# Performance work log

Measured on AMD Instinct MI355X. Metric: run time of the kernel, lower is better.

The kernel has to match this reference:

```python
import jax, jax.numpy as jnp
import numpy as np

N, E = 100000, 1600000
D_IN, D_H, D_OUT = 32, 64, 1


def _init_linear(key, fan_in, fan_out):
    k1, k2 = jax.random.split(key)
    lim = 1.0 / np.sqrt(fan_in)
    w = jax.random.uniform(k1, (fan_in, fan_out), minval=-lim, maxval=lim, dtype=jnp.float32)
    b = jax.random.uniform(k2, (fan_out,), minval=-lim, maxval=lim, dtype=jnp.float32)
    return w, b


def setup_inputs() -> dict:
    key = jax.random.key(0)
    ks = jax.random.split(key, 8)
    x = jax.random.normal(ks[0], (N, D_IN), dtype=jnp.float32)
    edge_index = jax.random.randint(ks[1], (2, E), 0, N, dtype=jnp.int64)
    w1_rel, b1 = _init_linear(ks[2], D_IN, D_H)
    w1_root, _ = _init_linear(ks[3], D_IN, D_H)
    w2_rel, b2 = _init_linear(ks[4], D_H, D_H)
    w2_root, _ = _init_linear(ks[5], D_H, D_H)
    w3_rel, b3 = _init_linear(ks[6], D_H, D_OUT)
    w3_root, _ = _init_linear(ks[7], D_H, D_OUT)
    return {
        "x": x,
        "w1_rel": w1_rel, "b1": b1, "w1_root": w1_root,
        "w2_rel": w2_rel, "b2": b2, "w2_root": w2_root,
        "w3_rel": w3_rel, "b3": b3, "w3_root": w3_root,
        "edge_index": edge_index,
    }


def _graph_conv(x, edge_index, w_rel, b_rel, w_root):
    # PyG GraphConv: out_i = W_rel @ (sum_{j->i} x_j) + b_rel + W_root @ x_i
    src, dst = edge_index[0], edge_index[1]
    agg = jax.ops.segment_sum(x[src], dst, num_segments=x.shape[0])  # [N, d]
    return agg @ w_rel + b_rel + x @ w_root


def reference(x, w1_rel, b1, w1_root, w2_rel, b2, w2_root, w3_rel, b3, w3_root, edge_index):
    # Dropout is inactive in eval mode (F.dropout with training=False is identity).
    h = jax.nn.relu(_graph_conv(x, edge_index, w1_rel, b1, w1_root))
    h = jax.nn.relu(_graph_conv(h, edge_index, w2_rel, b2, w2_root))
    out = _graph_conv(h, edge_index, w3_rel, b3, w3_root)
    return out.reshape(-1)  # [N], since output_dim == 1
```

## Files before the change

kernel.cpp:

```cpp
#include <hip/hip_runtime.h>
#include <hip/hip_fp16.h>

typedef _Float16 f16x8 __attribute__((ext_vector_type(8)));
typedef float    f32x4 __attribute__((ext_vector_type(4)));

constexpr int DIN = 32;
constexpr int DH  = 64;
constexpr int NBSHIFT = 8;
constexpr int TILE_A  = 4096;


__global__ __launch_bounds__(256) void k_zero512(int* __restrict__ p) {
  p[threadIdx.x] = 0;
  p[256 + threadIdx.x] = 0;
}

__global__ __launch_bounds__(256) void k_chist(
    const int* __restrict__ dst, int* __restrict__ ch, int E, int nbuckets) {
  __shared__ int hist[512];
  long long t0 = (long long)blockIdx.x * TILE_A;
  int cnt = (int)min((long long)TILE_A, (long long)E - t0);
  for (int i = threadIdx.x; i < nbuckets; i += 256) hist[i] = 0;
  __syncthreads();
  for (int r = threadIdx.x; r < cnt; r += 256)
    atomicAdd(&hist[dst[t0 + r] >> NBSHIFT], 1);
  __syncthreads();
  for (int i = threadIdx.x; i < nbuckets; i += 256)
    if (hist[i]) atomicAdd(&ch[i], hist[i]);
}

__global__ __launch_bounds__(256) void k_cscan(
    const int* __restrict__ ch, int* __restrict__ cb, int* __restrict__ bcur,
    int nbuckets, int E) {
  __shared__ int ts[256];
  int i0 = threadIdx.x * 2, i1 = i0 + 1;
  int v0 = (i0 < nbuckets) ? ch[i0] : 0;
  int v1 = (i1 < nbuckets) ? ch[i1] : 0;
  int s = v0 + v1;
  ts[threadIdx.x] = s;
  __syncthreads();
  for (int off = 1; off < 256; off <<= 1) {
    int val = (threadIdx.x >= off) ? ts[threadIdx.x - off] : 0;
    __syncthreads();
    ts[threadIdx.x] += val;
    __syncthreads();
  }
  int ex = ts[threadIdx.x] - s;
  if (i0 < nbuckets) { cb[i0] = ex;      bcur[i0] = ex; }
  if (i1 < nbuckets) { cb[i1] = ex + v0; bcur[i1] = ex + v0; }
  if (threadIdx.x == 255) cb[nbuckets] = E;
}

__global__ __launch_bounds__(256) void k_binA(
    const int* __restrict__ src, const int* __restrict__ dst,
    int* __restrict__ bcur, unsigned* __restrict__ bin,
    int E, int nbuckets) {
  __shared__ int hist[512];
  __shared__ int base[512];
  long long t0 = (long long)blockIdx.x * TILE_A;
  int cnt = (int)min((long long)TILE_A, (long long)E - t0);
  for (int i = threadIdx.x; i < nbuckets; i += 256) hist[i] = 0;
  __syncthreads();
  for (int r = threadIdx.x; r < cnt; r += 256)
    atomicAdd(&hist[dst[t0 + r] >> NBSHIFT], 1);
  __syncthreads();
  for (int i = threadIdx.x; i < nbuckets; i += 256) {
    int c = hist[i];
    base[i] = c ? atomicAdd(&bcur[i], c) : 0;
    hist[i] = 0;
  }
  __syncthreads();
  for (int r = threadIdx.x; r < cnt; r += 256) {
    int d = dst[t0 + r];
    int s = src[t0 + r];
    int b = d >> NBSHIFT;
    int off = atomicAdd(&hist[b], 1);
    bin[base[b] + off] = ((unsigned)(d & 255) << 17) | (unsigned)s;
  }
}

__global__ __launch_bounds__(256) void k_fillB(
    const unsigned* __restrict__ bin, const int* __restrict__ cb,
    int* __restrict__ rp, int* __restrict__ ssrc, int n, int E) {
  __shared__ int deg[256];
  __shared__ int ts[256];
  __shared__ int cur[256];
  int b = blockIdx.x;
  int nbase = b << NBSHIFT;
  int nn = min(256, n - nbase);
  int ebeg = cb[b], eend = cb[b + 1];
  deg[threadIdx.x] = 0;
  __syncthreads();
  for (int e = ebeg + (int)threadIdx.x; e < eend; e += 256)
    atomicAdd(&deg[bin[e] >> 17], 1);
  __syncthreads();
  int d = deg[threadIdx.x];
  ts[threadIdx.x] = d;
  __syncthreads();
  for (int off = 1; off < 256; off <<= 1) {
    int val = (threadIdx.x >= off) ? ts[threadIdx.x - off] : 0;
    __syncthreads();
    ts[threadIdx.x] += val;
    __syncthreads();
  }
  int pref = ts[threadIdx.x] - d;
  if ((int)threadIdx.x < nn) {
    rp[nbase + threadIdx.x] = ebeg + pref;
    cur[threadIdx.x] = ebeg + pref;
  }
  if (b == 0 && threadIdx.x == 0) rp[n] = E;
  __syncthreads();
  for (int e = ebeg + (int)threadIdx.x; e < eend; e += 256) {
    unsigned u = bin[e];
    int dlow = (int)(u >> 17);
    int s = (int)(u & 0x1FFFF);
    int pos = atomicAdd(&cur[dlow], 1);
    ssrc[pos] = s;
  }
}


__global__ __launch_bounds__(256) void k_tohalf(
    const float2* __restrict__ in, __half2* __restrict__ f1, int n2) {
  int i = blockIdx.x * 256 + threadIdx.x;
  if (i >= n2) return;
  float2 v = in[i];
  int node = i >> 4, f2 = i & 15;
  f1[(size_t)node * 32 + f2] = __floats2half2_rn(v.x, v.y);
}

template<int LOGG, int LDH8, int OFFR8, int OFFW8>
__global__ __launch_bounds__(256) void k_gather(
    const f16x8* __restrict__ feat, const int* __restrict__ rp,
    const int* __restrict__ ssrc, f16x8* __restrict__ outp, int n) {
  int t = blockIdx.x * 256 + threadIdx.x;
  int node = t >> LOGG;
  int f8 = t & ((1 << LOGG) - 1);
  if (node >= n) return;
  int beg = rp[node], end = rp[node + 1];
  float acc[8];
#pragma unroll
  for (int j = 0; j < 8; ++j) acc[j] = 0.f;
  int e = beg;
  for (; e + 3 < end; e += 4) {
    int s0 = ssrc[e];
    int s1 = ssrc[e + 1];
    int s2 = ssrc[e + 2];
    int s3 = ssrc[e + 3];
    f16x8 v0 = feat[(size_t)s0 * LDH8 + OFFR8 + f8];
    f16x8 v1 = feat[(size_t)s1 * LDH8 + OFFR8 + f8];
    f16x8 v2 = feat[(size_t)s2 * LDH8 + OFFR8 + f8];
    f16x8 v3 = feat[(size_t)s3 * LDH8 + OFFR8 + f8];
#pragma unroll
    for (int j = 0; j < 8; ++j) {
      acc[j] += (float)v0[j];
      acc[j] += (float)v1[j];
      acc[j] += (float)v2[j];
      acc[j] += (float)v3[j];
    }
  }
  for (; e < end; ++e) {
    f16x8 v = feat[(size_t)ssrc[e] * LDH8 + OFFR8 + f8];
#pragma unroll
    for (int j = 0; j < 8; ++j) acc[j] += (float)v[j];
  }
  f16x8 r;
#pragma unroll
  for (int j = 0; j < 8; ++j) r[j] = (_Float16)acc[j];
  outp[(size_t)node * LDH8 + OFFW8 + f8] = r;
}


__global__ __launch_bounds__(256) void k_prepw1(
    const float* __restrict__ w_rel, const float* __restrict__ w_root,
    __half* __restrict__ wf) {
  int u = blockIdx.x * 256 + threadIdx.x;
  if (u >= 512) return;
  int lane = u & 63, kt = (u >> 6) & 1, mt = u >> 7;
  int out = 16 * mt + (lane & 15);
  int kb = 32 * kt + (lane >> 4) * 8;
  union { uint4 q; __half h[8]; } pk;
#pragma unroll
  for (int j = 0; j < 8; ++j) {
    int k = kb + j;
    float w = (k < 32) ? w_root[k * DH + out] : w_rel[(k - 32) * DH + out];
    pk.h[j] = __float2half(w);
  }
  *(uint4*)(wf + (size_t)u * 8) = pk.q;
}

__global__ __launch_bounds__(256) void k_prepw2(
    const float* __restrict__ w_rel, const float* __restrict__ w_root,
    __half* __restrict__ wf) {
  int u = blockIdx.x * 256 + threadIdx.x;
  if (u >= 1024) return;
  int lane = u & 63, kt = (u >> 6) & 3, mt = u >> 8;
  int out = 16 * mt + (lane & 15);
  int kb = 32 * kt + (lane >> 4) * 8;
  union { uint4 q; __half h[8]; } pk;
#pragma unroll
  for (int j = 0; j < 8; ++j) {
    int k = kb + j;
    float w = (k < 64) ? w_rel[k * DH + out] : w_root[(k - 64) * DH + out];
    pk.h[j] = __float2half(w);
  }
  *(uint4*)(wf + (size_t)u * 8) = pk.q;
}

__global__ __launch_bounds__(256) void k_l1mfma(
    const _Float16* __restrict__ F1, const _Float16* __restrict__ WF,
    const float* __restrict__ b1, _Float16* __restrict__ F2, int n) {
  int lane = threadIdx.x & 63;
  int wv = (blockIdx.x * 256 + threadIdx.x) >> 6;
  int nb = wv * 16;
  if (nb >= n) return;
  int node = nb + (lane & 15);
  int nodeld = min(node, n - 1);
  const _Float16* fp = F1 + (size_t)nodeld * 64 + (lane >> 4) * 8;
  f16x8 bf[2];
#pragma unroll
  for (int kt = 0; kt < 2; ++kt) bf[kt] = *(const f16x8*)(fp + kt * 32);
  const f16x8* ap = (const f16x8*)WF + lane;
  f32x4 acc[4];
#pragma unroll
  for (int mt = 0; mt < 4; ++mt) acc[mt] = (f32x4)(0.f);
#pragma unroll
  for (int mt = 0; mt < 4; ++mt)
#pragma unroll
    for (int kt = 0; kt < 2; ++kt)
      acc[mt] = __builtin_amdgcn_mfma_f32_16x16x32_f16(
          ap[(mt * 2 + kt) * 64], bf[kt], acc[mt], 0, 0, 0);
  if (node >= n) return;
  int jb = (lane >> 4) * 4;
  _Float16* op = F2 + (size_t)node * 128 + 64 + jb;
#pragma unroll
  for (int mt = 0; mt < 4; ++mt) {
    f32x4 vb = *(const f32x4*)(b1 + 16 * mt + jb);
    union { uint2 u; _Float16 h[4]; } pk;
#pragma unroll
    for (int r = 0; r < 4; ++r)
      pk.h[r] = (_Float16)fmaxf(acc[mt][r] + vb[r], 0.f);
    *(uint2*)(op + 16 * mt) = pk.u;
  }
}

__global__ __launch_bounds__(256) void k_l2mfma(
    const _Float16* __restrict__ F2, const _Float16* __restrict__ WF,
    const float* __restrict__ b2, const float* __restrict__ w3rel,
    const float* __restrict__ w3root,
    float* __restrict__ S, float* __restrict__ T, int n) {
  int lane = threadIdx.x & 63;
  int wv = (blockIdx.x * 256 + threadIdx.x) >> 6;
  int nb = wv * 16;
  if (nb >= n) return;
  int node = nb + (lane & 15);
  int nodeld = min(node, n - 1);
  const _Float16* fp = F2 + (size_t)nodeld * 128 + (lane >> 4) * 8;
  f16x8 bf[4];
#pragma unroll
  for (int kt = 0; kt < 4; ++kt) bf[kt] = *(const f16x8*)(fp + kt * 32);
  const f16x8* ap = (const f16x8*)WF + lane;
  f32x4 acc[4];
#pragma unroll
  for (int mt = 0; mt < 4; ++mt) acc[mt] = (f32x4)(0.f);
#pragma unroll
  for (int mt = 0; mt < 4; ++mt)
#pragma unroll
    for (int kt = 0; kt < 4; ++kt)
      acc[mt] = __builtin_amdgcn_mfma_f32_16x16x32_f16(
          ap[(mt * 4 + kt) * 64], bf[kt], acc[mt], 0, 0, 0);
  int jb = (lane >> 4) * 4;
  float s = 0.f, t = 0.f;
#pragma unroll
  for (int mt = 0; mt < 4; ++mt) {
    f32x4 vb = *(const f32x4*)(b2 + 16 * mt + jb);
    f32x4 vr = *(const f32x4*)(w3rel + 16 * mt + jb);
    f32x4 vt = *(const f32x4*)(w3root + 16 * mt + jb);
#pragma unroll
    for (int r = 0; r < 4; ++r) {
      float h = fmaxf(acc[mt][r] + vb[r], 0.f);
      s = fmaf(h, vr[r], s);
      t = fmaf(h, vt[r], t);
    }
  }
  s += __shfl_xor(s, 16); s += __shfl_xor(s, 32);
  t += __shfl_xor(t, 16); t += __shfl_xor(t, 32);
  if (lane < 16 && node < n) { S[node] = s; T[node] = t; }
}


__global__ __launch_bounds__(256) void k_final(
    const float* __restrict__ sv, const int* __restrict__ rp,
    const int* __restrict__ ssrc, const float* __restrict__ T,
    const float* __restrict__ b3, float* __restrict__ out, int n) {
  int t = blockIdx.x * 256 + threadIdx.x;
  int node = t >> 2;
  int l = t & 3;
  if (node >= n) return;
  int beg = rp[node], end = rp[node + 1];
  float a = 0.f;
  for (int e = beg + l; e < end; e += 4) a += sv[ssrc[e]];
  a += __shfl_xor(a, 1);
  a += __shfl_xor(a, 2);
  if (l == 0) out[node] = a + b3[0] + T[node];
}


extern "C" void kernel_launch(void* const* d_in, const int* in_sizes, int n_in,
                              void* d_out, int out_size, void* d_ws, size_t ws_size,
                              hipStream_t stream) {
  const float* x       = (const float*)d_in[0];
  const float* w1_rel  = (const float*)d_in[1];
  const float* b1      = (const float*)d_in[2];
  const float* w1_root = (const float*)d_in[3];
  const float* w2_rel  = (const float*)d_in[4];
  const float* b2      = (const float*)d_in[5];
  const float* w2_root = (const float*)d_in[6];
  const float* w3_rel  = (const float*)d_in[7];
  const float* b3      = (const float*)d_in[8];
  const float* w3_root = (const float*)d_in[9];
  const int*   edge    = (const int*)d_in[10];

  const int n = in_sizes[0] / DIN;
  const int E = in_sizes[10] / 2;
  const int* src = edge;
  const int* dst = edge + E;

  _Float16* F1 = (_Float16*)d_ws;
  _Float16* F2 = F1 + (size_t)n * 64;
  float*    S  = (float*)(F2 + (size_t)n * 128);
  float*    T  = S + n;
  int* RP   = (int*)(T + n);
  int* SSRC = RP + ((n + 8) & ~7);
  int* CH   = SSRC + E;
  int* CB   = CH + 512;
  int* BCUR = CB + 520;
  __half* WF1 = (__half*)(BCUR + 512);
  __half* WF2 = WF1 + 4096;
  unsigned* BIN = (unsigned*)F2;

  const int B = 256;
  const int nbuckets = (n + 255) >> NBSHIFT;
  const int gA = (E + TILE_A - 1) / TILE_A;

  k_zero512<<<1, B, 0, stream>>>(CH);
  k_chist<<<gA, B, 0, stream>>>(dst, CH, E, nbuckets);
  k_cscan<<<1, B, 0, stream>>>(CH, CB, BCUR, nbuckets, E);
  k_binA<<<gA, B, 0, stream>>>(src, dst, BCUR, BIN, E, nbuckets);
  k_fillB<<<nbuckets, B, 0, stream>>>(BIN, CB, RP, SSRC, n, E);

  k_prepw1<<<2, B, 0, stream>>>(w1_rel, w1_root, WF1);
  k_prepw2<<<4, B, 0, stream>>>(w2_rel, w2_root, WF2);
  {
    int n2 = n * (DIN / 2);
    k_tohalf<<<(n2 + B - 1) / B, B, 0, stream>>>((const float2*)x, (__half2*)F1, n2);
  }

  {
    long long tot = (long long)n << 2;
    k_gather<2, 8, 0, 4><<<(unsigned)((tot + B - 1) / B), B, 0, stream>>>(
        (const f16x8*)F1, RP, SSRC, (f16x8*)F1, n);
  }
  {
    int waves = (n + 15) / 16;
    int blocks = (waves + 3) / 4;
    k_l1mfma<<<blocks, B, 0, stream>>>(F1, (const _Float16*)WF1, b1, F2, n);
  }

  {
    long long tot = (long long)n << 3;
    k_gather<3, 16, 8, 0><<<(unsigned)((tot + B - 1) / B), B, 0, stream>>>(
        (const f16x8*)F2, RP, SSRC, (f16x8*)F2, n);
  }
  {
    int waves = (n + 15) / 16;
    int blocks = (waves + 3) / 4;
    k_l2mfma<<<blocks, B, 0, stream>>>(F2, (const _Float16*)WF2,
                                       b2, w3_rel, w3_root, S, T, n);
  }

  k_final<<<(4 * n + B - 1) / B, B, 0, stream>>>(S, RP, SSRC, T, b3, (float*)d_out, n);
}
```

Measured before the change: 165.0 us.

## Fuse gather with MFMA per layer, merge setup kernels, sort bins in LDS

```diff
diff --git a/kernel.cpp b/kernel.cpp
--- a/kernel.cpp
+++ b/kernel.cpp
@@ -8,12 +8,55 @@
 constexpr int DH  = 64;
 constexpr int NBSHIFT = 8;
 constexpr int TILE_A  = 4096;
-
-
-__global__ __launch_bounds__(256) void k_zero512(int* __restrict__ p) {
-  p[threadIdx.x] = 0;
-  p[256 + threadIdx.x] = 0;
-}
+constexpr int FB_CAP  = 6144;
+
+
+__global__ __launch_bounds__(256) void k_setup(
+    const float2* __restrict__ x2, __half2* __restrict__ xh,
+    const float* __restrict__ w1_rel, const float* __restrict__ w1_root,
+    const float* __restrict__ w2_rel, const float* __restrict__ w2_root,
+    __half* __restrict__ wf1, __half* __restrict__ wf2,
+    int* __restrict__ ch, int n2) {
+  int i = blockIdx.x * 256 + threadIdx.x;
+  if (i < n2) {
+    float2 v = x2[i];
+    xh[i] = __floats2half2_rn(v.x, v.y);
+    return;
+  }
+  int u = i - n2;
+  if (u < 512) {
+    int lane = u & 63, kt = (u >> 6) & 1, mt = u >> 7;
+    int out = 16 * mt + (lane & 15);
+    int kb = 32 * kt + (lane >> 4) * 8;
+    union { uint4 q; __half h[8]; } pk;
+#pragma unroll
+    for (int j = 0; j < 8; ++j) {
+      int k = kb + j;
+      float w = (k < 32) ? w1_root[k * DH + out] : w1_rel[(k - 32) * DH + out];
+      pk.h[j] = __float2half(w);
+    }
+    *(uint4*)(wf1 + (size_t)u * 8) = pk.q;
+    return;
+  }
+  u -= 512;
+  if (u < 1024) {
+    int lane = u & 63, kt = (u >> 6) & 3, mt = u >> 8;
+    int out = 16 * mt + (lane & 15);
+    int kb = 32 * kt + (lane >> 4) * 8;
+    union { uint4 q; __half h[8]; } pk;
+#pragma unroll
+    for (int j = 0; j < 8; ++j) {
+      int k = kb + j;
+      float w = (k < 64) ? w2_rel[k * DH + out] : w2_root[(k - 64) * DH + out];
+      pk.h[j] = __float2half(w);
+    }
+    *(uint4*)(wf2 + (size_t)u * 8) = pk.q;
+    return;
+  }
+  u -= 1024;
+  if (u < 512) ch[u] = 0;
+}
+
 
 __global__ __launch_bounds__(256) void k_chist(
     const int* __restrict__ dst, int* __restrict__ ch, int E, int nbuckets) {
@@ -56,26 +99,63 @@
     int* __restrict__ bcur, unsigned* __restrict__ bin,
     int E, int nbuckets) {
   __shared__ int hist[512];
-  __shared__ int base[512];
+  __shared__ int lbase[512];
+  __shared__ int gbase[512];
+  __shared__ int ts[256];
+  __shared__ unsigned lsort[TILE_A];
+  __shared__ unsigned short lbuck[TILE_A];
   long long t0 = (long long)blockIdx.x * TILE_A;
   int cnt = (int)min((long long)TILE_A, (long long)E - t0);
-  for (int i = threadIdx.x; i < nbuckets; i += 256) hist[i] = 0;
-  __syncthreads();
-  for (int r = threadIdx.x; r < cnt; r += 256)
-    atomicAdd(&hist[dst[t0 + r] >> NBSHIFT], 1);
-  __syncthreads();
-  for (int i = threadIdx.x; i < nbuckets; i += 256) {
-    int c = hist[i];
-    base[i] = c ? atomicAdd(&bcur[i], c) : 0;
-    hist[i] = 0;
-  }
-  __syncthreads();
-  for (int r = threadIdx.x; r < cnt; r += 256) {
-    int d = dst[t0 + r];
-    int s = src[t0 + r];
-    int b = d >> NBSHIFT;
-    int off = atomicAdd(&hist[b], 1);
-    bin[base[b] + off] = ((unsigned)(d & 255) << 17) | (unsigned)s;
+  for (int i = threadIdx.x; i < 512; i += 256) hist[i] = 0;
+  __syncthreads();
+  unsigned pk[TILE_A / 256];
+  int bo[TILE_A / 256];
+#pragma unroll
+  for (int q = 0; q < TILE_A / 256; ++q) {
+    int r = (int)threadIdx.x + q * 256;
+    if (r < cnt) {
+      int d = dst[t0 + r];
+      int s = src[t0 + r];
+      int b = d >> NBSHIFT;
+      int off = atomicAdd(&hist[b], 1);
+      pk[q] = ((unsigned)(d & 255) << 17) | (unsigned)s;
+      bo[q] = (b << 16) | off;
+    }
+  }
+  __syncthreads();
+  {
+    int i0 = threadIdx.x * 2, i1 = i0 + 1;
+    int v0 = hist[i0], v1 = hist[i1];
+    int s2 = v0 + v1;
+    ts[threadIdx.x] = s2;
+    __syncthreads();
+    for (int off = 1; off < 256; off <<= 1) {
+      int val = (threadIdx.x >= off) ? ts[threadIdx.x - off] : 0;
+      __syncthreads();
+      ts[threadIdx.x] += val;
+      __syncthreads();
+    }
+    int ex = ts[threadIdx.x] - s2;
+    lbase[i0] = ex;
+    lbase[i1] = ex + v0;
+    gbase[i0] = v0 ? atomicAdd(&bcur[i0], v0) : 0;
+    gbase[i1] = v1 ? atomicAdd(&bcur[i1], v1) : 0;
+  }
+  __syncthreads();
+#pragma unroll
+  for (int q = 0; q < TILE_A / 256; ++q) {
+    int r = (int)threadIdx.x + q * 256;
+    if (r < cnt) {
+      int b = bo[q] >> 16, off = bo[q] & 0xFFFF;
+      int li = lbase[b] + off;
+      lsort[li] = pk[q];
+      lbuck[li] = (unsigned short)b;
+    }
+  }
+  __syncthreads();
+  for (int i = threadIdx.x; i < cnt; i += 256) {
+    int b = lbuck[i];
+    bin[gbase[b] + (i - lbase[b])] = lsort[i];
   }
 }
 
@@ -85,10 +165,12 @@
   __shared__ int deg[256];
   __shared__ int ts[256];
   __shared__ int cur[256];
+  __shared__ int lsort[FB_CAP];
   int b = blockIdx.x;
   int nbase = b << NBSHIFT;
   int nn = min(256, n - nbase);
   int ebeg = cb[b], eend = cb[b + 1];
+  int cnt = eend - ebeg;
   deg[threadIdx.x] = 0;
   __syncthreads();
   for (int e = ebeg + (int)threadIdx.x; e < eend; e += 256)
@@ -104,161 +186,161 @@
     __syncthreads();
   }
   int pref = ts[threadIdx.x] - d;
-  if ((int)threadIdx.x < nn) {
-    rp[nbase + threadIdx.x] = ebeg + pref;
-    cur[threadIdx.x] = ebeg + pref;
-  }
+  if ((int)threadIdx.x < nn) rp[nbase + threadIdx.x] = ebeg + pref;
   if (b == 0 && threadIdx.x == 0) rp[n] = E;
-  __syncthreads();
-  for (int e = ebeg + (int)threadIdx.x; e < eend; e += 256) {
-    unsigned u = bin[e];
-    int dlow = (int)(u >> 17);
-    int s = (int)(u & 0x1FFFF);
-    int pos = atomicAdd(&cur[dlow], 1);
-    ssrc[pos] = s;
-  }
-}
-
-
-__global__ __launch_bounds__(256) void k_tohalf(
-    const float2* __restrict__ in, __half2* __restrict__ f1, int n2) {
-  int i = blockIdx.x * 256 + threadIdx.x;
-  if (i >= n2) return;
-  float2 v = in[i];
-  int node = i >> 4, f2 = i & 15;
-  f1[(size_t)node * 32 + f2] = __floats2half2_rn(v.x, v.y);
-}
-
-template<int LOGG, int LDH8, int OFFR8, int OFFW8>
-__global__ __launch_bounds__(256) void k_gather(
-    const f16x8* __restrict__ feat, const int* __restrict__ rp,
-    const int* __restrict__ ssrc, f16x8* __restrict__ outp, int n) {
-  int t = blockIdx.x * 256 + threadIdx.x;
-  int node = t >> LOGG;
-  int f8 = t & ((1 << LOGG) - 1);
-  if (node >= n) return;
-  int beg = rp[node], end = rp[node + 1];
-  float acc[8];
-#pragma unroll
-  for (int j = 0; j < 8; ++j) acc[j] = 0.f;
-  int e = beg;
-  for (; e + 3 < end; e += 4) {
-    int s0 = ssrc[e];
-    int s1 = ssrc[e + 1];
-    int s2 = ssrc[e + 2];
-    int s3 = ssrc[e + 3];
-    f16x8 v0 = feat[(size_t)s0 * LDH8 + OFFR8 + f8];
-    f16x8 v1 = feat[(size_t)s1 * LDH8 + OFFR8 + f8];
-    f16x8 v2 = feat[(size_t)s2 * LDH8 + OFFR8 + f8];
-    f16x8 v3 = feat[(size_t)s3 * LDH8 + OFFR8 + f8];
-#pragma unroll
-    for (int j = 0; j < 8; ++j) {
-      acc[j] += (float)v0[j];
-      acc[j] += (float)v1[j];
-      acc[j] += (float)v2[j];
-      acc[j] += (float)v3[j];
-    }
-  }
-  for (; e < end; ++e) {
-    f16x8 v = feat[(size_t)ssrc[e] * LDH8 + OFFR8 + f8];
-#pragma unroll
-    for (int j = 0; j < 8; ++j) acc[j] += (float)v[j];
-  }
-  f16x8 r;
-#pragma unroll
-  for (int j = 0; j < 8; ++j) r[j] = (_Float16)acc[j];
-  outp[(size_t)node * LDH8 + OFFW8 + f8] = r;
-}
-
-
-__global__ __launch_bounds__(256) void k_prepw1(
-    const float* __restrict__ w_rel, const float* __restrict__ w_root,
-    __half* __restrict__ wf) {
-  int u = blockIdx.x * 256 + threadIdx.x;
-  if (u >= 512) return;
-  int lane = u & 63, kt = (u >> 6) & 1, mt = u >> 7;
-  int out = 16 * mt + (lane & 15);
-  int kb = 32 * kt + (lane >> 4) * 8;
-  union { uint4 q; __half h[8]; } pk;
-#pragma unroll
-  for (int j = 0; j < 8; ++j) {
-    int k = kb + j;
-    float w = (k < 32) ? w_root[k * DH + out] : w_rel[(k - 32) * DH + out];
-    pk.h[j] = __float2half(w);
-  }
-  *(uint4*)(wf + (size_t)u * 8) = pk.q;
-}
-
-__global__ __launch_bounds__(256) void k_prepw2(
-    const float* __restrict__ w_rel, const float* __restrict__ w_root,
-    __half* __restrict__ wf) {
-  int u = blockIdx.x * 256 + threadIdx.x;
-  if (u >= 1024) return;
-  int lane = u & 63, kt = (u >> 6) & 3, mt = u >> 8;
-  int out = 16 * mt + (lane & 15);
-  int kb = 32 * kt + (lane >> 4) * 8;
-  union { uint4 q; __half h[8]; } pk;
-#pragma unroll
-  for (int j = 0; j < 8; ++j) {
-    int k = kb + j;
-    float w = (k < 64) ? w_rel[k * DH + out] : w_root[(k - 64) * DH + out];
-    pk.h[j] = __float2half(w);
-  }
-  *(uint4*)(wf + (size_t)u * 8) = pk.q;
-}
-
-__global__ __launch_bounds__(256) void k_l1mfma(
-    const _Float16* __restrict__ F1, const _Float16* __restrict__ WF,
-    const float* __restrict__ b1, _Float16* __restrict__ F2, int n) {
-  int lane = threadIdx.x & 63;
-  int wv = (blockIdx.x * 256 + threadIdx.x) >> 6;
-  int nb = wv * 16;
-  if (nb >= n) return;
-  int node = nb + (lane & 15);
+  cur[threadIdx.x] = pref;
+  __syncthreads();
+  if (cnt <= FB_CAP) {
+    for (int e = ebeg + (int)threadIdx.x; e < eend; e += 256) {
+      unsigned u = bin[e];
+      int pos = atomicAdd(&cur[u >> 17], 1);
+      lsort[pos] = (int)(u & 0x1FFFF);
+    }
+    __syncthreads();
+    for (int i = threadIdx.x; i < cnt; i += 256)
+      ssrc[ebeg + i] = lsort[i];
+  } else {
+    for (int e = ebeg + (int)threadIdx.x; e < eend; e += 256) {
+      unsigned u = bin[e];
+      int pos = atomicAdd(&cur[u >> 17], 1);
+      ssrc[ebeg + pos] = (int)(u & 0x1FFFF);
+    }
+  }
+}
+
+__global__ __launch_bounds__(256) void k_l1fused(
+    const _Float16* __restrict__ X, const int* __restrict__ rp,
+    const int* __restrict__ ssrc, const _Float16* __restrict__ WF,
+    const float* __restrict__ b1, _Float16* __restrict__ H1, int n) {
+  __shared__ _Float16 sagg[64][40];
+  int tid = threadIdx.x;
+  int nl = tid >> 2;
+  int unit = tid & 3;
+  int nodeg = blockIdx.x * 64 + nl;
+  {
+    float acc[8];
+#pragma unroll
+    for (int j = 0; j < 8; ++j) acc[j] = 0.f;
+    if (nodeg < n) {
+      int beg = rp[nodeg], end = rp[nodeg + 1];
+      const f16x8* fx = (const f16x8*)X;
+      int e = beg;
+      for (; e + 3 < end; e += 4) {
+        int s0 = ssrc[e], s1 = ssrc[e + 1], s2 = ssrc[e + 2], s3 = ssrc[e + 3];
+        f16x8 v0 = fx[(size_t)s0 * 4 + unit];
+        f16x8 v1 = fx[(size_t)s1 * 4 + unit];
+        f16x8 v2 = fx[(size_t)s2 * 4 + unit];
+        f16x8 v3 = fx[(size_t)s3 * 4 + unit];
+#pragma unroll
+        for (int j = 0; j < 8; ++j) {
+          acc[j] += (float)v0[j]; acc[j] += (float)v1[j];
+          acc[j] += (float)v2[j]; acc[j] += (float)v3[j];
+        }
+      }
+      for (; e < end; ++e) {
+        f16x8 v = fx[(size_t)ssrc[e] * 4 + unit];
+#pragma unroll
+        for (int j = 0; j < 8; ++j) acc[j] += (float)v[j];
+      }
+    }
+    f16x8 r;
+#pragma unroll
+    for (int j = 0; j < 8; ++j) r[j] = (_Float16)acc[j];
+    *(f16x8*)&sagg[nl][unit * 8] = r;
+  }
+  __syncthreads();
+  int lane = tid & 63;
+  int w = tid >> 6;
+  int nl16 = w * 16 + (lane & 15);
+  int node = blockIdx.x * 64 + nl16;
   int nodeld = min(node, n - 1);
-  const _Float16* fp = F1 + (size_t)nodeld * 64 + (lane >> 4) * 8;
-  f16x8 bf[2];
-#pragma unroll
-  for (int kt = 0; kt < 2; ++kt) bf[kt] = *(const f16x8*)(fp + kt * 32);
+  f16x8 bf0 = *(const f16x8*)(X + (size_t)nodeld * 32 + (lane >> 4) * 8);
+  f16x8 bf1 = *(const f16x8*)&sagg[nl16][(lane >> 4) * 8];
   const f16x8* ap = (const f16x8*)WF + lane;
   f32x4 acc[4];
 #pragma unroll
   for (int mt = 0; mt < 4; ++mt) acc[mt] = (f32x4)(0.f);
 #pragma unroll
-  for (int mt = 0; mt < 4; ++mt)
-#pragma unroll
-    for (int kt = 0; kt < 2; ++kt)
-      acc[mt] = __builtin_amdgcn_mfma_f32_16x16x32_f16(
-          ap[(mt * 2 + kt) * 64], bf[kt], acc[mt], 0, 0, 0);
+  for (int mt = 0; mt < 4; ++mt) {
+    acc[mt] = __builtin_amdgcn_mfma_f32_16x16x32_f16(ap[(mt * 2 + 0) * 64], bf0, acc[mt], 0, 0, 0);
+    acc[mt] = __builtin_amdgcn_mfma_f32_16x16x32_f16(ap[(mt * 2 + 1) * 64], bf1, acc[mt], 0, 0, 0);
+  }
   if (node >= n) return;
   int jb = (lane >> 4) * 4;
-  _Float16* op = F2 + (size_t)node * 128 + 64 + jb;
+  _Float16* op = H1 + (size_t)node * 64 + jb;
 #pragma unroll
   for (int mt = 0; mt < 4; ++mt) {
     f32x4 vb = *(const f32x4*)(b1 + 16 * mt + jb);
-    union { uint2 u; _Float16 h[4]; } pk;
+    union { uint2 u2; _Float16 h[4]; } pko;
 #pragma unroll
     for (int r = 0; r < 4; ++r)
-      pk.h[r] = (_Float16)fmaxf(acc[mt][r] + vb[r], 0.f);
-    *(uint2*)(op + 16 * mt) = pk.u;
-  }
-}
-
-__global__ __launch_bounds__(256) void k_l2mfma(
-    const _Float16* __restrict__ F2, const _Float16* __restrict__ WF,
+      pko.h[r] = (_Float16)fmaxf(acc[mt][r] + vb[r], 0.f);
+    *(uint2*)(op + 16 * mt) = pko.u2;
+  }
+}
+
+__global__ __launch_bounds__(256) void k_l2fused(
+    const _Float16* __restrict__ H1, const int* __restrict__ rp,
+    const int* __restrict__ ssrc, const _Float16* __restrict__ WF,
     const float* __restrict__ b2, const float* __restrict__ w3rel,
     const float* __restrict__ w3root,
     float* __restrict__ S, float* __restrict__ T, int n) {
-  int lane = threadIdx.x & 63;
-  int wv = (blockIdx.x * 256 + threadIdx.x) >> 6;
-  int nb = wv * 16;
-  if (nb >= n) return;
-  int node = nb + (lane & 15);
+  __shared__ _Float16 sagg[64][72];
+  int tid = threadIdx.x;
+  int nl = tid >> 2;
+  int u0 = tid & 3;
+  int nodeg = blockIdx.x * 64 + nl;
+  {
+    float acc[16];
+#pragma unroll
+    for (int j = 0; j < 16; ++j) acc[j] = 0.f;
+    if (nodeg < n) {
+      int beg = rp[nodeg], end = rp[nodeg + 1];
+      const f16x8* fh = (const f16x8*)H1;
+      int e = beg;
+      for (; e + 1 < end; e += 2) {
+        int s0 = ssrc[e], s1 = ssrc[e + 1];
+        f16x8 a0 = fh[(size_t)s0 * 8 + u0];
+        f16x8 c0 = fh[(size_t)s0 * 8 + u0 + 4];
+        f16x8 a1 = fh[(size_t)s1 * 8 + u0];
+        f16x8 c1 = fh[(size_t)s1 * 8 + u0 + 4];
+#pragma unroll
+        for (int j = 0; j < 8; ++j) {
+          acc[j] += (float)a0[j];     acc[j] += (float)a1[j];
+          acc[8 + j] += (float)c0[j]; acc[8 + j] += (float)c1[j];
+        }
+      }
+      for (; e < end; ++e) {
+        int s0 = ssrc[e];
+        f16x8 a0 = fh[(size_t)s0 * 8 + u0];
+        f16x8 c0 = fh[(size_t)s0 * 8 + u0 + 4];
+#pragma unroll
+        for (int j = 0; j < 8; ++j) {
+          acc[j] += (float)a0[j];
+          acc[8 + j] += (float)c0[j];
+        }
+      }
+    }
+    f16x8 r0, r1;
+#pragma unroll
+    for (int j = 0; j < 8; ++j) {
+      r0[j] = (_Float16)acc[j];
+      r1[j] = (_Float16)acc[8 + j];
+    }
+    *(f16x8*)&sagg[nl][u0 * 8] = r0;
+    *(f16x8*)&sagg[nl][(u0 + 4) * 8] = r1;
+  }
+  __syncthreads();
+  int lane = tid & 63;
+  int w = tid >> 6;
+  int nl16 = w * 16 + (lane & 15);
+  int node = blockIdx.x * 64 + nl16;
   int nodeld = min(node, n - 1);
-  const _Float16* fp = F2 + (size_t)nodeld * 128 + (lane >> 4) * 8;
   f16x8 bf[4];
-#pragma unroll
-  for (int kt = 0; kt < 4; ++kt) bf[kt] = *(const f16x8*)(fp + kt * 32);
+  bf[0] = *(const f16x8*)&sagg[nl16][(lane >> 4) * 8];
+  bf[1] = *(const f16x8*)&sagg[nl16][32 + (lane >> 4) * 8];
+  bf[2] = *(const f16x8*)(H1 + (size_t)nodeld * 64 + (lane >> 4) * 8);
+  bf[3] = *(const f16x8*)(H1 + (size_t)nodeld * 64 + 32 + (lane >> 4) * 8);
   const f16x8* ap = (const f16x8*)WF + lane;
   f32x4 acc[4];
 #pragma unroll
@@ -326,9 +408,9 @@
   const int* src = edge;
   const int* dst = edge + E;
 
-  _Float16* F1 = (_Float16*)d_ws;
-  _Float16* F2 = F1 + (size_t)n * 64;
-  float*    S  = (float*)(F2 + (size_t)n * 128);
+  _Float16* XH = (_Float16*)d_ws;
+  _Float16* H1 = XH + (size_t)n * 32;
+  float*    S  = (float*)(H1 + (size_t)n * 64);
   float*    T  = S + n;
   int* RP   = (int*)(T + n);
   int* SSRC = RP + ((n + 8) & ~7);
@@ -337,47 +419,29 @@
   int* BCUR = CB + 520;
   __half* WF1 = (__half*)(BCUR + 512);
   __half* WF2 = WF1 + 4096;
-  unsigned* BIN = (unsigned*)F2;
+  unsigned* BIN = (unsigned*)H1;
 
   const int B = 256;
   const int nbuckets = (n + 255) >> NBSHIFT;
   const int gA = (E + TILE_A - 1) / TILE_A;
-
-  k_zero512<<<1, B, 0, stream>>>(CH);
+  const int gF = (n + 63) / 64;
+
+  {
+    int n2 = n * 16;
+    int tot = n2 + 2048;
+    k_setup<<<(tot + B - 1) / B, B, 0, stream>>>(
+        (const float2*)x, (__half2*)XH, w1_rel, w1_root, w2_rel, w2_root,
+        WF1, WF2, CH, n2);
+  }
+
   k_chist<<<gA, B, 0, stream>>>(dst, CH, E, nbuckets);
   k_cscan<<<1, B, 0, stream>>>(CH, CB, BCUR, nbuckets, E);
   k_binA<<<gA, B, 0, stream>>>(src, dst, BCUR, BIN, E, nbuckets);
   k_fillB<<<nbuckets, B, 0, stream>>>(BIN, CB, RP, SSRC, n, E);
 
-  k_prepw1<<<2, B, 0, stream>>>(w1_rel, w1_root, WF1);
-  k_prepw2<<<4, B, 0, stream>>>(w2_rel, w2_root, WF2);
-  {
-    int n2 = n * (DIN / 2);
-    k_tohalf<<<(n2 + B - 1) / B, B, 0, stream>>>((const float2*)x, (__half2*)F1, n2);
-  }
-
-  {
-    long long tot = (long long)n << 2;
-    k_gather<2, 8, 0, 4><<<(unsigned)((tot + B - 1) / B), B, 0, stream>>>(
-        (const f16x8*)F1, RP, SSRC, (f16x8*)F1, n);
-  }
-  {
-    int waves = (n + 15) / 16;
-    int blocks = (waves + 3) / 4;
-    k_l1mfma<<<blocks, B, 0, stream>>>(F1, (const _Float16*)WF1, b1, F2, n);
-  }
-
-  {
-    long long tot = (long long)n << 3;
-    k_gather<3, 16, 8, 0><<<(unsigned)((tot + B - 1) / B), B, 0, stream>>>(
-        (const f16x8*)F2, RP, SSRC, (f16x8*)F2, n);
-  }
-  {
-    int waves = (n + 15) / 16;
-    int blocks = (waves + 3) / 4;
-    k_l2mfma<<<blocks, B, 0, stream>>>(F2, (const _Float16*)WF2,
-                                       b2, w3_rel, w3_root, S, T, n);
-  }
+  k_l1fused<<<gF, B, 0, stream>>>(XH, RP, SSRC, (const _Float16*)WF1, b1, H1, n);
+  k_l2fused<<<gF, B, 0, stream>>>(H1, RP, SSRC, (const _Float16*)WF2,
+                                  b2, w3_rel, w3_root, S, T, n);
 
   k_final<<<(4 * n + B - 1) / B, B, 0, stream>>>(S, RP, SSRC, T, b3, (float*)d_out, n);
 }
```

Measured after the change: 143.0 us. 1.15x faster.
